# Kernel tuning notes

Hardware: AMD Instinct MI355X
Metric: run time of the kernel (lower is better)

## Reference

```python
import jax, jax.numpy as jnp
import numpy as np

B, T, D_MODEL, N_HEADS = 2, 2048, 1024, 16
HEAD_DIM = D_MODEL // N_HEADS


def _ln(x, g, b, eps=1e-5):
    m = x.mean(-1, keepdims=True)
    v = ((x - m) ** 2).mean(-1, keepdims=True)
    return (x - m) / jnp.sqrt(v + eps) * g + b


def setup_inputs() -> dict:
    key = jax.random.key(0)
    ks = jax.random.split(key, 7)
    f = jnp.float32
    x = jax.random.normal(ks[0], (B, T, D_MODEL), f)
    Wq = jax.random.normal(ks[1], (D_MODEL, D_MODEL), f) * 0.02
    Wk = jax.random.normal(ks[2], (D_MODEL, D_MODEL), f) * 0.02
    Wv = jax.random.normal(ks[3], (D_MODEL, D_MODEL), f) * 0.02
    Wo = jax.random.normal(ks[4], (D_MODEL, D_MODEL), f) * 0.02
    return {
        'x': x, 'Wq': Wq, 'Wk': Wk, 'Wv': Wv, 'Wo': Wo,
        'evolution_rate': jnp.asarray(0.1, f),
        'memory_decay': jnp.asarray(0.85, f),
        'temporal_weights': jax.random.normal(ks[5], (HEAD_DIM,), f) * 0.02,
        'q_gamma': jnp.ones((HEAD_DIM,), f), 'q_beta': jnp.zeros((HEAD_DIM,), f),
        'k_gamma': jnp.ones((HEAD_DIM,), f), 'k_beta': jnp.zeros((HEAD_DIM,), f),
    }


def reference(x, Wq, Wk, Wv, Wo, evolution_rate, memory_decay,
              temporal_weights, q_gamma, q_beta, k_gamma, k_beta):
    b, t, c = x.shape
    h, d = N_HEADS, HEAD_DIM
    # projections (torch Linear: y = x @ W^T), split heads -> [B,H,T,D]
    q = jnp.einsum('btc,oc->bto', x, Wq).reshape(b, t, h, d).transpose(0, 2, 1, 3)
    k = jnp.einsum('btc,oc->bto', x, Wk).reshape(b, t, h, d).transpose(0, 2, 1, 3)
    v = jnp.einsum('btc,oc->bto', x, Wv).reshape(b, t, h, d).transpose(0, 2, 1, 3)

    sig_md = jax.nn.sigmoid(memory_decay)
    # temporal signal per position: sin(sigmoid(er)*(pos+1) * w)  -> [T,D]
    ef = jax.nn.sigmoid(evolution_rate) * jnp.arange(1, t + 1, dtype=x.dtype)
    ts = jnp.sin(ef[:, None] * temporal_weights[None, :])

    def step(mem, inp):  # mem: [B,H,D]
        q_t, k_t, ts_t = inp  # [B,H,D],[B,H,D],[D]
        eq = _ln(q_t + ts_t + sig_md * mem, q_gamma, q_beta)
        ek = _ln(k_t + 0.5 * ts_t + 0.3 * sig_md * mem, k_gamma, k_beta)
        return 0.7 * mem + 0.3 * q_t, (eq, ek)

    mem0 = jnp.zeros((b, h, d), x.dtype)
    qT = q.transpose(2, 0, 1, 3)  # [T,B,H,D]
    kT = k.transpose(2, 0, 1, 3)
    _, (eqT, ekT) = jax.lax.scan(step, mem0, (qT, kT, ts))
    eq = eqT.transpose(1, 2, 0, 3)  # [B,H,T,D]
    ek = ekT.transpose(1, 2, 0, 3)

    scale = 1.0 / np.sqrt(d).astype(np.float32)
    scores = jnp.einsum('bhtd,bhsd->bhts', eq, ek) * scale
    causal = jnp.tril(jnp.ones((t, t), bool))
    scores = jnp.where(causal[None, None], scores, -jnp.inf)
    w = jax.nn.softmax(scores, axis=-1)  # dropout is identity (eval)
    out = jnp.einsum('bhts,bhsd->bhtd', w, v)
    out = out.transpose(0, 2, 1, 3).reshape(b, t, c)
    return jnp.einsum('btc,oc->bto', out, Wo)
```

## Files before the change

### kernel.cpp

```cpp
#include <hip/hip_runtime.h>
#include <stdint.h>

#define T_SEQ   2048
#define NHEADS  16
#define HDIM    64
#define DMODEL  1024

typedef __attribute__((ext_vector_type(8))) _Float16 half8_t;
typedef __attribute__((ext_vector_type(4))) float    float4_t;

typedef __attribute__((address_space(1))) unsigned char ga_u8;
typedef __attribute__((address_space(3))) unsigned char lds_u8;

__device__ __forceinline__ unsigned short f2h(float f) {
  _Float16 h = (_Float16)f;
  return __builtin_bit_cast(unsigned short, h);
}
__device__ __forceinline__ unsigned packh2(float a, float b) {
  return (unsigned)f2h(a) | ((unsigned)f2h(b) << 16);
}
__device__ __forceinline__ unsigned packu2(unsigned short a, unsigned short b) {
  return (unsigned)a | ((unsigned)b << 16);
}
__device__ __forceinline__ void async_copy16(const void* g, void* l) {
  __builtin_amdgcn_global_load_lds((ga_u8*)g, (lds_u8*)l, 16, 0, 0);
}

__global__ __launch_bounds__(256) void cvt_f32_f16(const float* __restrict__ s,
                                                   unsigned short* __restrict__ d, int n4) {
  int i = blockIdx.x * 256 + threadIdx.x;
  if (i >= n4) return;
  float4 v = ((const float4*)s)[i];
  ushort4 o;
  o.x = f2h(v.x); o.y = f2h(v.y); o.z = f2h(v.z); o.w = f2h(v.w);
  ((ushort4*)d)[i] = o;
}

__global__ __launch_bounds__(256) void cvt_weights(
    const float* __restrict__ w0, const float* __restrict__ w1,
    const float* __restrict__ w2, const float* __restrict__ w3,
    unsigned short* __restrict__ d0, unsigned short* __restrict__ d1,
    unsigned short* __restrict__ d2, unsigned short* __restrict__ d3, int n4) {
  int i = blockIdx.x * 256 + threadIdx.x;
  if (i >= n4) return;
  const float* s = (blockIdx.y == 0) ? w0 : (blockIdx.y == 1) ? w1 : (blockIdx.y == 2) ? w2 : w3;
  unsigned short* d = (blockIdx.y == 0) ? d0 : (blockIdx.y == 1) ? d1 : (blockIdx.y == 2) ? d2 : d3;
  float4 v = ((const float4*)s)[i];
  ushort4 o;
  o.x = f2h(v.x); o.y = f2h(v.y); o.z = f2h(v.z); o.w = f2h(v.w);
  ((ushort4*)d)[i] = o;
}

__device__ __forceinline__ void storeC(float* p, float v) { *p = v; }
__device__ __forceinline__ void storeC(unsigned short* p, float v) { *p = f2h(v); }

template <typename OutT>
__global__ __launch_bounds__(256) void gemm_nt_f16(const unsigned short* __restrict__ A,
                                                   const unsigned short* __restrict__ B,
                                                   OutT* __restrict__ C) {
  __shared__ alignas(16) unsigned short As[128 * 32];
  __shared__ alignas(16) unsigned short Bs[128 * 32];
  const int tid  = threadIdx.x;
  const int lane = tid & 63, w = tid >> 6;
  const int c = lane & 15, g = lane >> 4;
  const int wr = w >> 1, wc = w & 1;
  const int m0 = blockIdx.y * 128, n0 = blockIdx.x * 128;

  float4_t acc[4][4];
#pragma unroll
  for (int m = 0; m < 4; ++m)
#pragma unroll
    for (int n = 0; n < 4; ++n) acc[m][n] = (float4_t){0.f, 0.f, 0.f, 0.f};

  for (int k0 = 0; k0 < 1024; k0 += 32) {
    __syncthreads();
#pragma unroll
    for (int r = 0; r < 2; ++r) {
      const int idx = r * 256 + tid;
      const int row = idx >> 2, kc = (idx & 3) * 8;
      async_copy16(A + (size_t)(m0 + row) * 1024 + k0 + kc, As + r * 2048 + w * 512);
      async_copy16(B + (size_t)(n0 + row) * 1024 + k0 + kc, Bs + r * 2048 + w * 512);
    }
    __syncthreads();
    half8_t af[4], bf[4];
#pragma unroll
    for (int m = 0; m < 4; ++m) af[m] = *(const half8_t*)&As[(wr * 64 + m * 16 + c) * 32 + g * 8];
#pragma unroll
    for (int n = 0; n < 4; ++n) bf[n] = *(const half8_t*)&Bs[(wc * 64 + n * 16 + c) * 32 + g * 8];
#pragma unroll
    for (int m = 0; m < 4; ++m)
#pragma unroll
      for (int n = 0; n < 4; ++n)
        acc[m][n] = __builtin_amdgcn_mfma_f32_16x16x32_f16(af[m], bf[n], acc[m][n], 0, 0, 0);
  }
#pragma unroll
  for (int m = 0; m < 4; ++m)
#pragma unroll
    for (int j = 0; j < 4; ++j) {
      const int row = m0 + wr * 64 + m * 16 + g * 4 + j;
#pragma unroll
      for (int n = 0; n < 4; ++n) {
        const int col = n0 + wc * 64 + n * 16 + c;
        storeC(C + (size_t)row * 1024 + col, acc[m][n][j]);
      }
    }
}

__global__ __launch_bounds__(64) void evolve_ln_f32(
    const float* __restrict__ q, const float* __restrict__ k,
    const float* __restrict__ er_p, const float* __restrict__ md_p,
    const float* __restrict__ tw, const float* __restrict__ qgamma,
    const float* __restrict__ qbeta, const float* __restrict__ kgamma,
    const float* __restrict__ kbeta,
    unsigned short* __restrict__ eq, unsigned short* __restrict__ ek) {
  const int lane = threadIdx.x;
  const int t0 = blockIdx.x * 32;
  const int bh = blockIdx.y;
  const int b = bh >> 4, h = bh & 15;
  const float sig_er = 1.f / (1.f + expf(-er_p[0]));
  const float smd    = 1.f / (1.f + expf(-md_p[0]));
  const float wv = tw[lane];
  const float gq = qgamma[lane], bq = qbeta[lane];
  const float gk = kgamma[lane], bk = kbeta[lane];
  const size_t base = ((size_t)b * T_SEQ) * DMODEL + h * HDIM + lane;

  float mem = 0.f;
  const int start = (t0 >= 64) ? (t0 - 64) : 0;
  for (int t = start; t < t0; ++t)
    mem = 0.7f * mem + 0.3f * q[base + (size_t)t * DMODEL];

  for (int t = t0; t < t0 + 32; ++t) {
    const float qv = q[base + (size_t)t * DMODEL];
    const float kv = k[base + (size_t)t * DMODEL];
    const float ts = sinf(sig_er * (float)(t + 1) * wv);
    const float xq = qv + ts + smd * mem;
    const float xk = kv + 0.5f * ts + 0.3f * smd * mem;
    float s1 = xq, s2 = xq * xq, s3 = xk, s4 = xk * xk;
#pragma unroll
    for (int off = 32; off > 0; off >>= 1) {
      s1 += __shfl_xor(s1, off);
      s2 += __shfl_xor(s2, off);
      s3 += __shfl_xor(s3, off);
      s4 += __shfl_xor(s4, off);
    }
    const float mq = s1 * (1.f / 64.f);
    const float vq = fmaxf(s2 * (1.f / 64.f) - mq * mq, 0.f);
    const float mk = s3 * (1.f / 64.f);
    const float vk = fmaxf(s4 * (1.f / 64.f) - mk * mk, 0.f);
    eq[base + (size_t)t * DMODEL] = f2h((xq - mq) * rsqrtf(vq + 1e-5f) * gq + bq);
    ek[base + (size_t)t * DMODEL] = f2h((xk - mk) * rsqrtf(vk + 1e-5f) * gk + bk);
    mem = 0.7f * mem + 0.3f * qv;
  }
}

__global__ __launch_bounds__(256) void attn_fused(
    const unsigned short* __restrict__ eq, const unsigned short* __restrict__ ek,
    const unsigned short* __restrict__ v, unsigned short* __restrict__ o) {
  __shared__ alignas(16) float Ssh[4][16][36];
  __shared__ float Alds[4][16];
  __shared__ float Llds[4][16];
  const int tid = threadIdx.x;
  const int lane = tid & 63, w = tid >> 6;
  const int c = lane & 15, g = lane >> 4;
  const int p = blockIdx.x * 4 + w;
  const int bh = blockIdx.y;
  const int b = bh >> 4, h = bh & 15;
  const size_t head = ((size_t)b * T_SEQ) * DMODEL + h * HDIM;

  for (int half = 0; half < 2; ++half) {
    const int sub = half ? (127 - p) : p;
    const int qw = sub * 16;
    const int qrow = qw + c;

    const half8_t aq0 = *(const half8_t*)(eq + head + (size_t)qrow * DMODEL + g * 8);
    const half8_t aq1 = *(const half8_t*)(eq + head + (size_t)qrow * DMODEL + 32 + g * 8);

    float4_t acc[4];
#pragma unroll
    for (int n = 0; n < 4; ++n) acc[n] = (float4_t){0.f, 0.f, 0.f, 0.f};
    float mrun = -1e30f, lsum = 0.f;

    const int ntiles = (qw >> 5) + 1;
    for (int tile = 0; tile < ntiles; ++tile) {
      const int s0 = tile * 32;
#pragma unroll
      for (int st = 0; st < 2; ++st) {
        const unsigned short* ekr = ek + head + (size_t)(s0 + st * 16 + c) * DMODEL;
        const half8_t bk0 = *(const half8_t*)(ekr + g * 8);
        const half8_t bk1 = *(const half8_t*)(ekr + 32 + g * 8);
        float4_t z = (float4_t){0.f, 0.f, 0.f, 0.f};
        z = __builtin_amdgcn_mfma_f32_16x16x32_f16(aq0, bk0, z, 0, 0, 0);
        z = __builtin_amdgcn_mfma_f32_16x16x32_f16(aq1, bk1, z, 0, 0, 0);
#pragma unroll
        for (int j = 0; j < 4; ++j)
          Ssh[w][g * 4 + j][st * 16 + c] = z[j] * 0.125f;
      }

      float pf[8];
      float tmax = -1e30f;
#pragma unroll
      for (int e = 0; e < 8; ++e) {
        const int sa = s0 + g * 8 + e;
        const float val = (sa <= qrow) ? Ssh[w][c][g * 8 + e] : -1e30f;
        pf[e] = val;
        tmax = fmaxf(tmax, val);
      }
      tmax = fmaxf(tmax, __shfl_xor(tmax, 16));
      tmax = fmaxf(tmax, __shfl_xor(tmax, 32));
      const float mnew = fmaxf(mrun, tmax);
      const float alpha = __expf(mrun - mnew);
      mrun = mnew;
      float psum = 0.f;
#pragma unroll
      for (int e = 0; e < 8; ++e) {
        pf[e] = __expf(pf[e] - mnew);
        psum += pf[e];
      }
      psum += __shfl_xor(psum, 16);
      psum += __shfl_xor(psum, 32);
      lsum = lsum * alpha + psum;
      if (g == 0) Alds[w][c] = alpha;

      uint4 pu;
      pu.x = packh2(pf[0], pf[1]);
      pu.y = packh2(pf[2], pf[3]);
      pu.z = packh2(pf[4], pf[5]);
      pu.w = packh2(pf[6], pf[7]);
      const half8_t pa = __builtin_bit_cast(half8_t, pu);

      float af[4];
#pragma unroll
      for (int j = 0; j < 4; ++j) af[j] = Alds[w][g * 4 + j];
#pragma unroll
      for (int n = 0; n < 4; ++n) {
        acc[n][0] *= af[0]; acc[n][1] *= af[1];
        acc[n][2] *= af[2]; acc[n][3] *= af[3];
      }
      const unsigned short* vp = v + head + (size_t)(s0 + g * 8) * DMODEL + c;
#pragma unroll
      for (int n = 0; n < 4; ++n) {
        const unsigned short* vq2 = vp + n * 16;
        uint4 bu;
        bu.x = packu2(vq2[0 * DMODEL], vq2[1 * DMODEL]);
        bu.y = packu2(vq2[2 * DMODEL], vq2[3 * DMODEL]);
        bu.z = packu2(vq2[4 * DMODEL], vq2[5 * DMODEL]);
        bu.w = packu2(vq2[6 * DMODEL], vq2[7 * DMODEL]);
        const half8_t bv = __builtin_bit_cast(half8_t, bu);
        acc[n] = __builtin_amdgcn_mfma_f32_16x16x32_f16(pa, bv, acc[n], 0, 0, 0);
      }
    }

    if (g == 0) Llds[w][c] = lsum;
    float lj[4];
#pragma unroll
    for (int j = 0; j < 4; ++j) lj[j] = 1.f / Llds[w][g * 4 + j];
#pragma unroll
    for (int n = 0; n < 4; ++n)
#pragma unroll
      for (int j = 0; j < 4; ++j)
        o[head + (size_t)(qw + g * 4 + j) * DMODEL + n * 16 + c] = f2h(acc[n][j] * lj[j]);
  }
}

extern "C" void kernel_launch(void* const* d_in, const int* in_sizes, int n_in,
                              void* d_out, int out_size, void* d_ws, size_t ws_size,
                              hipStream_t stream) {
  const float* x  = (const float*)d_in[0];
  const float* Wq = (const float*)d_in[1];
  const float* Wk = (const float*)d_in[2];
  const float* Wv = (const float*)d_in[3];
  const float* Wo = (const float*)d_in[4];
  const float* er = (const float*)d_in[5];
  const float* md = (const float*)d_in[6];
  const float* tw = (const float*)d_in[7];
  const float* qg = (const float*)d_in[8];
  const float* qb = (const float*)d_in[9];
  const float* kg = (const float*)d_in[10];
  const float* kb = (const float*)d_in[11];

  const size_t NX = (size_t)2 * T_SEQ * DMODEL;
  const size_t NW = (size_t)DMODEL * DMODEL;

  unsigned short* xh  = (unsigned short*)d_ws;
  unsigned short* woh = xh + NX;
  unsigned short* wqh = woh + NW;
  unsigned short* wkh = wqh + NW;
  unsigned short* wvh = wkh + NW;
  float* qf  = (float*)(wvh + NW);
  float* kf  = qf + NX;
  unsigned short* ekh = (unsigned short*)(kf + NX);
  unsigned short* vh  = ekh + NX;
  unsigned short* eqh = xh;
  unsigned short* aoh = (unsigned short*)kf;

  const int n4x = (int)(NX / 4), n4w = (int)(NW / 4);

  cvt_f32_f16<<<n4x / 256, 256, 0, stream>>>(x, xh, n4x);
  cvt_weights<<<dim3(n4w / 256, 4), 256, 0, stream>>>(Wq, Wk, Wv, Wo,
                                                      wqh, wkh, wvh, woh, n4w);

  dim3 ggrid(DMODEL / 128, (2 * T_SEQ) / 128);
  gemm_nt_f16<float><<<ggrid, 256, 0, stream>>>(xh, wqh, qf);
  gemm_nt_f16<float><<<ggrid, 256, 0, stream>>>(xh, wkh, kf);
  gemm_nt_f16<unsigned short><<<ggrid, 256, 0, stream>>>(xh, wvh, vh);

  evolve_ln_f32<<<dim3(T_SEQ / 32, 32), 64, 0, stream>>>(qf, kf, er, md, tw,
                                                         qg, qb, kg, kb, eqh, ekh);

  attn_fused<<<dim3(16, 32), 256, 0, stream>>>(eqh, ekh, vh, aoh);

  gemm_nt_f16<float><<<ggrid, 256, 0, stream>>>(aoh, woh, (float*)d_out);
}
```

Baseline: 252.3 us.

## Pre-transpose V and widen attention KV tiles to 64

Adds a kernel that transposes V per head into a [D,T] layout, so the attention PV MFMA operand loads become contiguous 16-byte vector loads instead of eight strided scalar gathers. It also doubles the KV tile from 32 to 64 keys, halving the softmax rescale and reduction overhead per key. The cost is an extra kernel launch and one extra pass over V in memory, plus higher register and LDS use per wave.

```diff
diff --git a/kernel.cpp b/kernel.cpp
--- a/kernel.cpp
+++ b/kernel.cpp
@@ -153,10 +153,42 @@
   }
 }
 
+__global__ __launch_bounds__(256) void transpose_v(const unsigned short* __restrict__ v,
+                                                   unsigned short* __restrict__ vt) {
+  __shared__ alignas(16) unsigned short tile[64][72];
+  const int tid = threadIdx.x;
+  const int t0 = blockIdx.x * 64;
+  const int bh = blockIdx.y;
+  const int b = bh >> 4, h = bh & 15;
+  const size_t src = ((size_t)b * T_SEQ + t0) * DMODEL + h * HDIM;
+
+  const int r = tid >> 2, c0 = (tid & 3) * 16;
+  const int sw = ((r >> 4) & 3) << 4;
+  const uint4 a0 = *(const uint4*)(v + src + (size_t)r * DMODEL + c0);
+  const uint4 a1 = *(const uint4*)(v + src + (size_t)r * DMODEL + c0 + 8);
+  *(uint4*)&tile[r][c0 ^ sw] = a0;
+  *(uint4*)&tile[r][(c0 ^ sw) + 8] = a1;
+  __syncthreads();
+
+  const int dr = tid >> 2, tc = (tid & 3) * 16;
+  const int swr = ((tc >> 4) & 3) << 4;
+  unsigned short tmp[16];
+#pragma unroll
+  for (int j = 0; j < 16; ++j) tmp[j] = tile[tc + j][dr ^ swr];
+  uint4 o0, o1;
+  o0.x = packu2(tmp[0], tmp[1]);   o0.y = packu2(tmp[2], tmp[3]);
+  o0.z = packu2(tmp[4], tmp[5]);   o0.w = packu2(tmp[6], tmp[7]);
+  o1.x = packu2(tmp[8], tmp[9]);   o1.y = packu2(tmp[10], tmp[11]);
+  o1.z = packu2(tmp[12], tmp[13]); o1.w = packu2(tmp[14], tmp[15]);
+  const size_t dst = (size_t)bh * HDIM * T_SEQ + (size_t)dr * T_SEQ + t0 + tc;
+  *(uint4*)(vt + dst) = o0;
+  *(uint4*)(vt + dst + 8) = o1;
+}
+
 __global__ __launch_bounds__(256) void attn_fused(
     const unsigned short* __restrict__ eq, const unsigned short* __restrict__ ek,
-    const unsigned short* __restrict__ v, unsigned short* __restrict__ o) {
-  __shared__ alignas(16) float Ssh[4][16][36];
+    const unsigned short* __restrict__ vt, unsigned short* __restrict__ o) {
+  __shared__ alignas(16) float Ssh[4][16][68];
   __shared__ float Alds[4][16];
   __shared__ float Llds[4][16];
   const int tid = threadIdx.x;
@@ -165,7 +197,8 @@
   const int p = blockIdx.x * 4 + w;
   const int bh = blockIdx.y;
   const int b = bh >> 4, h = bh & 15;
-  const size_t head = ((size_t)b * T_SEQ) * DMODEL + h * HDIM;
+  const size_t head  = ((size_t)b * T_SEQ) * DMODEL + h * HDIM;
+  const size_t headt = (size_t)bh * HDIM * T_SEQ;
 
   for (int half = 0; half < 2; ++half) {
     const int sub = half ? (127 - p) : p;
@@ -180,11 +213,11 @@
     for (int n = 0; n < 4; ++n) acc[n] = (float4_t){0.f, 0.f, 0.f, 0.f};
     float mrun = -1e30f, lsum = 0.f;
 
-    const int ntiles = (qw >> 5) + 1;
+    const int ntiles = (qw >> 6) + 1;
     for (int tile = 0; tile < ntiles; ++tile) {
-      const int s0 = tile * 32;
-#pragma unroll
-      for (int st = 0; st < 2; ++st) {
+      const int s0 = tile * 64;
+#pragma unroll
+      for (int st = 0; st < 4; ++st) {
         const unsigned short* ekr = ek + head + (size_t)(s0 + st * 16 + c) * DMODEL;
         const half8_t bk0 = *(const half8_t*)(ekr + g * 8);
         const half8_t bk1 = *(const half8_t*)(ekr + 32 + g * 8);
@@ -196,14 +229,16 @@
           Ssh[w][g * 4 + j][st * 16 + c] = z[j] * 0.125f;
       }
 
-      float pf[8];
+      float pf[16];
       float tmax = -1e30f;
 #pragma unroll
       for (int e = 0; e < 8; ++e) {
-        const int sa = s0 + g * 8 + e;
-        const float val = (sa <= qrow) ? Ssh[w][c][g * 8 + e] : -1e30f;
-        pf[e] = val;
-        tmax = fmaxf(tmax, val);
+        const int sa0 = s0 + g * 8 + e;
+        const int sa1 = sa0 + 32;
+        const float v0 = (sa0 <= qrow) ? Ssh[w][c][g * 8 + e] : -1e30f;
+        const float v1 = (sa1 <= qrow) ? Ssh[w][c][32 + g * 8 + e] : -1e30f;
+        pf[e] = v0; pf[8 + e] = v1;
+        tmax = fmaxf(tmax, fmaxf(v0, v1));
       }
       tmax = fmaxf(tmax, __shfl_xor(tmax, 16));
       tmax = fmaxf(tmax, __shfl_xor(tmax, 32));
@@ -212,7 +247,7 @@
       mrun = mnew;
       float psum = 0.f;
 #pragma unroll
-      for (int e = 0; e < 8; ++e) {
+      for (int e = 0; e < 16; ++e) {
         pf[e] = __expf(pf[e] - mnew);
         psum += pf[e];
       }
@@ -221,12 +256,13 @@
       lsum = lsum * alpha + psum;
       if (g == 0) Alds[w][c] = alpha;
 
-      uint4 pu;
-      pu.x = packh2(pf[0], pf[1]);
-      pu.y = packh2(pf[2], pf[3]);
-      pu.z = packh2(pf[4], pf[5]);
-      pu.w = packh2(pf[6], pf[7]);
-      const half8_t pa = __builtin_bit_cast(half8_t, pu);
+      uint4 pu0, pu1;
+      pu0.x = packh2(pf[0], pf[1]);   pu0.y = packh2(pf[2], pf[3]);
+      pu0.z = packh2(pf[4], pf[5]);   pu0.w = packh2(pf[6], pf[7]);
+      pu1.x = packh2(pf[8], pf[9]);   pu1.y = packh2(pf[10], pf[11]);
+      pu1.z = packh2(pf[12], pf[13]); pu1.w = packh2(pf[14], pf[15]);
+      const half8_t pa0 = __builtin_bit_cast(half8_t, pu0);
+      const half8_t pa1 = __builtin_bit_cast(half8_t, pu1);
 
       float af[4];
 #pragma unroll
@@ -236,17 +272,13 @@
         acc[n][0] *= af[0]; acc[n][1] *= af[1];
         acc[n][2] *= af[2]; acc[n][3] *= af[3];
       }
-      const unsigned short* vp = v + head + (size_t)(s0 + g * 8) * DMODEL + c;
 #pragma unroll
       for (int n = 0; n < 4; ++n) {
-        const unsigned short* vq2 = vp + n * 16;
-        uint4 bu;
-        bu.x = packu2(vq2[0 * DMODEL], vq2[1 * DMODEL]);
-        bu.y = packu2(vq2[2 * DMODEL], vq2[3 * DMODEL]);
-        bu.z = packu2(vq2[4 * DMODEL], vq2[5 * DMODEL]);
-        bu.w = packu2(vq2[6 * DMODEL], vq2[7 * DMODEL]);
-        const half8_t bv = __builtin_bit_cast(half8_t, bu);
-        acc[n] = __builtin_amdgcn_mfma_f32_16x16x32_f16(pa, bv, acc[n], 0, 0, 0);
+        const unsigned short* vr = vt + headt + (size_t)(n * 16 + c) * T_SEQ + s0;
+        const half8_t bv0 = *(const half8_t*)(vr + g * 8);
+        const half8_t bv1 = *(const half8_t*)(vr + 32 + g * 8);
+        acc[n] = __builtin_amdgcn_mfma_f32_16x16x32_f16(pa0, bv0, acc[n], 0, 0, 0);
+        acc[n] = __builtin_amdgcn_mfma_f32_16x16x32_f16(pa1, bv1, acc[n], 0, 0, 0);
       }
     }
 
@@ -291,6 +323,7 @@
   unsigned short* ekh = (unsigned short*)(kf + NX);
   unsigned short* vh  = ekh + NX;
   unsigned short* eqh = xh;
+  unsigned short* vth = (unsigned short*)qf;
   unsigned short* aoh = (unsigned short*)kf;
 
   const int n4x = (int)(NX / 4), n4w = (int)(NW / 4);
@@ -307,7 +340,9 @@
   evolve_ln_f32<<<dim3(T_SEQ / 32, 32), 64, 0, stream>>>(qf, kf, er, md, tw,
                                                          qg, qb, kg, kb, eqh, ekh);
 
-  attn_fused<<<dim3(16, 32), 256, 0, stream>>>(eqh, ekh, vh, aoh);
+  transpose_v<<<dim3(T_SEQ / 64, 32), 256, 0, stream>>>(vh, vth);
+
+  attn_fused<<<dim3(16, 32), 256, 0, stream>>>(eqh, ekh, vth, aoh);
 
   gemm_nt_f16<float><<<ggrid, 256, 0, stream>>>(aoh, woh, (float*)d_out);
 }
```

Measured after the change: 298.0 us. 18.1% more time.

## Batch QKV GEMMs into one launch, store Q/K in fp16, split attention grid

Applied to the files above, without the earlier changes.

Merges the three projection GEMMs into one launch that uses blockIdx.z to pick the weight, and writes Q and K as fp16 instead of fp32, so evolve_ln reads half the bytes. The attention kernel drops its paired causal-balancing loop: each wave now handles a single 16-row query tile, and the grid is doubled to 32 blocks. This cuts launch count and memory traffic and raises parallelism. The cost is fp16 rounding of Q/K before the LayerNorm and possible load imbalance, since causal tiles now carry unequal work.

```diff
diff --git a/kernel.cpp b/kernel.cpp
--- a/kernel.cpp
+++ b/kernel.cpp
@@ -15,6 +15,9 @@
 __device__ __forceinline__ unsigned short f2h(float f) {
   _Float16 h = (_Float16)f;
   return __builtin_bit_cast(unsigned short, h);
+}
+__device__ __forceinline__ float h2f(unsigned short u) {
+  return (float)__builtin_bit_cast(_Float16, u);
 }
 __device__ __forceinline__ unsigned packh2(float a, float b) {
   return (unsigned)f2h(a) | ((unsigned)f2h(b) << 16);
@@ -51,13 +54,15 @@
   ((ushort4*)d)[i] = o;
 }
 
-__device__ __forceinline__ void storeC(float* p, float v) { *p = v; }
-__device__ __forceinline__ void storeC(unsigned short* p, float v) { *p = f2h(v); }
-
-template <typename OutT>
-__global__ __launch_bounds__(256) void gemm_nt_f16(const unsigned short* __restrict__ A,
-                                                   const unsigned short* __restrict__ B,
-                                                   OutT* __restrict__ C) {
+__global__ __launch_bounds__(256) void gemm_qkv(
+    const unsigned short* __restrict__ A,
+    const unsigned short* __restrict__ Bq, const unsigned short* __restrict__ Bk,
+    const unsigned short* __restrict__ Bv,
+    unsigned short* __restrict__ Cq, unsigned short* __restrict__ Ck,
+    unsigned short* __restrict__ Cv) {
+  const unsigned short* B = (blockIdx.z == 0) ? Bq : (blockIdx.z == 1) ? Bk : Bv;
+  unsigned short*       C = (blockIdx.z == 0) ? Cq : (blockIdx.z == 1) ? Ck : Cv;
+
   __shared__ alignas(16) unsigned short As[128 * 32];
   __shared__ alignas(16) unsigned short Bs[128 * 32];
   const int tid  = threadIdx.x;
@@ -101,13 +106,64 @@
 #pragma unroll
       for (int n = 0; n < 4; ++n) {
         const int col = n0 + wc * 64 + n * 16 + c;
-        storeC(C + (size_t)row * 1024 + col, acc[m][n][j]);
+        C[(size_t)row * 1024 + col] = f2h(acc[m][n][j]);
       }
     }
 }
 
-__global__ __launch_bounds__(64) void evolve_ln_f32(
-    const float* __restrict__ q, const float* __restrict__ k,
+__global__ __launch_bounds__(256) void gemm_nt_out(const unsigned short* __restrict__ A,
+                                                   const unsigned short* __restrict__ B,
+                                                   float* __restrict__ C) {
+  __shared__ alignas(16) unsigned short As[128 * 32];
+  __shared__ alignas(16) unsigned short Bs[128 * 32];
+  const int tid  = threadIdx.x;
+  const int lane = tid & 63, w = tid >> 6;
+  const int c = lane & 15, g = lane >> 4;
+  const int wr = w >> 1, wc = w & 1;
+  const int m0 = blockIdx.y * 128, n0 = blockIdx.x * 128;
+
+  float4_t acc[4][4];
+#pragma unroll
+  for (int m = 0; m < 4; ++m)
+#pragma unroll
+    for (int n = 0; n < 4; ++n) acc[m][n] = (float4_t){0.f, 0.f, 0.f, 0.f};
+
+  for (int k0 = 0; k0 < 1024; k0 += 32) {
+    __syncthreads();
+#pragma unroll
+    for (int r = 0; r < 2; ++r) {
+      const int idx = r * 256 + tid;
+      const int row = idx >> 2, kc = (idx & 3) * 8;
+      async_copy16(A + (size_t)(m0 + row) * 1024 + k0 + kc, As + r * 2048 + w * 512);
+      async_copy16(B + (size_t)(n0 + row) * 1024 + k0 + kc, Bs + r * 2048 + w * 512);
+    }
+    __syncthreads();
+    half8_t af[4], bf[4];
+#pragma unroll
+    for (int m = 0; m < 4; ++m) af[m] = *(const half8_t*)&As[(wr * 64 + m * 16 + c) * 32 + g * 8];
+#pragma unroll
+    for (int n = 0; n < 4; ++n) bf[n] = *(const half8_t*)&Bs[(wc * 64 + n * 16 + c) * 32 + g * 8];
+#pragma unroll
+    for (int m = 0; m < 4; ++m)
+#pragma unroll
+      for (int n = 0; n < 4; ++n)
+        acc[m][n] = __builtin_amdgcn_mfma_f32_16x16x32_f16(af[m], bf[n], acc[m][n], 0, 0, 0);
+  }
+#pragma unroll
+  for (int m = 0; m < 4; ++m)
+#pragma unroll
+    for (int j = 0; j < 4; ++j) {
+      const int row = m0 + wr * 64 + m * 16 + g * 4 + j;
+#pragma unroll
+      for (int n = 0; n < 4; ++n) {
+        const int col = n0 + wc * 64 + n * 16 + c;
+        C[(size_t)row * 1024 + col] = acc[m][n][j];
+      }
+    }
+}
+
+__global__ __launch_bounds__(64) void evolve_ln(
+    const unsigned short* __restrict__ q, const unsigned short* __restrict__ k,
     const float* __restrict__ er_p, const float* __restrict__ md_p,
     const float* __restrict__ tw, const float* __restrict__ qgamma,
     const float* __restrict__ qbeta, const float* __restrict__ kgamma,
@@ -127,11 +183,11 @@
   float mem = 0.f;
   const int start = (t0 >= 64) ? (t0 - 64) : 0;
   for (int t = start; t < t0; ++t)
-    mem = 0.7f * mem + 0.3f * q[base + (size_t)t * DMODEL];
+    mem = 0.7f * mem + 0.3f * h2f(q[base + (size_t)t * DMODEL]);
 
   for (int t = t0; t < t0 + 32; ++t) {
-    const float qv = q[base + (size_t)t * DMODEL];
-    const float kv = k[base + (size_t)t * DMODEL];
+    const float qv = h2f(q[base + (size_t)t * DMODEL]);
+    const float kv = h2f(k[base + (size_t)t * DMODEL]);
     const float ts = sinf(sig_er * (float)(t + 1) * wv);
     const float xq = qv + ts + smd * mem;
     const float xk = kv + 0.5f * ts + 0.3f * smd * mem;
@@ -162,104 +218,101 @@
   const int tid = threadIdx.x;
   const int lane = tid & 63, w = tid >> 6;
   const int c = lane & 15, g = lane >> 4;
-  const int p = blockIdx.x * 4 + w;
+  const int sub = blockIdx.x * 4 + w;
   const int bh = blockIdx.y;
   const int b = bh >> 4, h = bh & 15;
   const size_t head = ((size_t)b * T_SEQ) * DMODEL + h * HDIM;
 
-  for (int half = 0; half < 2; ++half) {
-    const int sub = half ? (127 - p) : p;
-    const int qw = sub * 16;
-    const int qrow = qw + c;
-
-    const half8_t aq0 = *(const half8_t*)(eq + head + (size_t)qrow * DMODEL + g * 8);
-    const half8_t aq1 = *(const half8_t*)(eq + head + (size_t)qrow * DMODEL + 32 + g * 8);
-
-    float4_t acc[4];
-#pragma unroll
-    for (int n = 0; n < 4; ++n) acc[n] = (float4_t){0.f, 0.f, 0.f, 0.f};
-    float mrun = -1e30f, lsum = 0.f;
-
-    const int ntiles = (qw >> 5) + 1;
-    for (int tile = 0; tile < ntiles; ++tile) {
-      const int s0 = tile * 32;
-#pragma unroll
-      for (int st = 0; st < 2; ++st) {
-        const unsigned short* ekr = ek + head + (size_t)(s0 + st * 16 + c) * DMODEL;
-        const half8_t bk0 = *(const half8_t*)(ekr + g * 8);
-        const half8_t bk1 = *(const half8_t*)(ekr + 32 + g * 8);
-        float4_t z = (float4_t){0.f, 0.f, 0.f, 0.f};
-        z = __builtin_amdgcn_mfma_f32_16x16x32_f16(aq0, bk0, z, 0, 0, 0);
-        z = __builtin_amdgcn_mfma_f32_16x16x32_f16(aq1, bk1, z, 0, 0, 0);
-#pragma unroll
-        for (int j = 0; j < 4; ++j)
-          Ssh[w][g * 4 + j][st * 16 + c] = z[j] * 0.125f;
-      }
-
-      float pf[8];
-      float tmax = -1e30f;
-#pragma unroll
-      for (int e = 0; e < 8; ++e) {
-        const int sa = s0 + g * 8 + e;
-        const float val = (sa <= qrow) ? Ssh[w][c][g * 8 + e] : -1e30f;
-        pf[e] = val;
-        tmax = fmaxf(tmax, val);
-      }
-      tmax = fmaxf(tmax, __shfl_xor(tmax, 16));
-      tmax = fmaxf(tmax, __shfl_xor(tmax, 32));
-      const float mnew = fmaxf(mrun, tmax);
-      const float alpha = __expf(mrun - mnew);
-      mrun = mnew;
-      float psum = 0.f;
-#pragma unroll
-      for (int e = 0; e < 8; ++e) {
-        pf[e] = __expf(pf[e] - mnew);
-        psum += pf[e];
-      }
-      psum += __shfl_xor(psum, 16);
-      psum += __shfl_xor(psum, 32);
-      lsum = lsum * alpha + psum;
-      if (g == 0) Alds[w][c] = alpha;
-
-      uint4 pu;
-      pu.x = packh2(pf[0], pf[1]);
-      pu.y = packh2(pf[2], pf[3]);
-      pu.z = packh2(pf[4], pf[5]);
-      pu.w = packh2(pf[6], pf[7]);
-      const half8_t pa = __builtin_bit_cast(half8_t, pu);
-
-      float af[4];
-#pragma unroll
-      for (int j = 0; j < 4; ++j) af[j] = Alds[w][g * 4 + j];
-#pragma unroll
-      for (int n = 0; n < 4; ++n) {
-        acc[n][0] *= af[0]; acc[n][1] *= af[1];
-        acc[n][2] *= af[2]; acc[n][3] *= af[3];
-      }
-      const unsigned short* vp = v + head + (size_t)(s0 + g * 8) * DMODEL + c;
-#pragma unroll
-      for (int n = 0; n < 4; ++n) {
-        const unsigned short* vq2 = vp + n * 16;
-        uint4 bu;
-        bu.x = packu2(vq2[0 * DMODEL], vq2[1 * DMODEL]);
-        bu.y = packu2(vq2[2 * DMODEL], vq2[3 * DMODEL]);
-        bu.z = packu2(vq2[4 * DMODEL], vq2[5 * DMODEL]);
-        bu.w = packu2(vq2[6 * DMODEL], vq2[7 * DMODEL]);
-        const half8_t bv = __builtin_bit_cast(half8_t, bu);
-        acc[n] = __builtin_amdgcn_mfma_f32_16x16x32_f16(pa, bv, acc[n], 0, 0, 0);
-      }
-    }
-
-    if (g == 0) Llds[w][c] = lsum;
-    float lj[4];
-#pragma unroll
-    for (int j = 0; j < 4; ++j) lj[j] = 1.f / Llds[w][g * 4 + j];
-#pragma unroll
-    for (int n = 0; n < 4; ++n)
+  const int qw = sub * 16;
+  const int qrow = qw + c;
+
+  const half8_t aq0 = *(const half8_t*)(eq + head + (size_t)qrow * DMODEL + g * 8);
+  const half8_t aq1 = *(const half8_t*)(eq + head + (size_t)qrow * DMODEL + 32 + g * 8);
+
+  float4_t acc[4];
+#pragma unroll
+  for (int n = 0; n < 4; ++n) acc[n] = (float4_t){0.f, 0.f, 0.f, 0.f};
+  float mrun = -1e30f, lsum = 0.f;
+
+  const int ntiles = (qw >> 5) + 1;
+  for (int tile = 0; tile < ntiles; ++tile) {
+    const int s0 = tile * 32;
+#pragma unroll
+    for (int st = 0; st < 2; ++st) {
+      const unsigned short* ekr = ek + head + (size_t)(s0 + st * 16 + c) * DMODEL;
+      const half8_t bk0 = *(const half8_t*)(ekr + g * 8);
+      const half8_t bk1 = *(const half8_t*)(ekr + 32 + g * 8);
+      float4_t z = (float4_t){0.f, 0.f, 0.f, 0.f};
+      z = __builtin_amdgcn_mfma_f32_16x16x32_f16(aq0, bk0, z, 0, 0, 0);
+      z = __builtin_amdgcn_mfma_f32_16x16x32_f16(aq1, bk1, z, 0, 0, 0);
 #pragma unroll
       for (int j = 0; j < 4; ++j)
-        o[head + (size_t)(qw + g * 4 + j) * DMODEL + n * 16 + c] = f2h(acc[n][j] * lj[j]);
+        Ssh[w][g * 4 + j][st * 16 + c] = z[j] * 0.125f;
+    }
+
+    float pf[8];
+    float tmax = -1e30f;
+#pragma unroll
+    for (int e = 0; e < 8; ++e) {
+      const int sa = s0 + g * 8 + e;
+      const float val = (sa <= qrow) ? Ssh[w][c][g * 8 + e] : -1e30f;
+      pf[e] = val;
+      tmax = fmaxf(tmax, val);
+    }
+    tmax = fmaxf(tmax, __shfl_xor(tmax, 16));
+    tmax = fmaxf(tmax, __shfl_xor(tmax, 32));
+    const float mnew = fmaxf(mrun, tmax);
+    const float alpha = __expf(mrun - mnew);
+    mrun = mnew;
+    float psum = 0.f;
+#pragma unroll
+    for (int e = 0; e < 8; ++e) {
+      pf[e] = __expf(pf[e] - mnew);
+      psum += pf[e];
+    }
+    psum += __shfl_xor(psum, 16);
+    psum += __shfl_xor(psum, 32);
+    lsum = lsum * alpha + psum;
+    if (g == 0) Alds[w][c] = alpha;
+
+    uint4 pu;
+    pu.x = packh2(pf[0], pf[1]);
+    pu.y = packh2(pf[2], pf[3]);
+    pu.z = packh2(pf[4], pf[5]);
+    pu.w = packh2(pf[6], pf[7]);
+    const half8_t pa = __builtin_bit_cast(half8_t, pu);
+
+    float af[4];
+#pragma unroll
+    for (int j = 0; j < 4; ++j) af[j] = Alds[w][g * 4 + j];
+#pragma unroll
+    for (int n = 0; n < 4; ++n) {
+      acc[n][0] *= af[0]; acc[n][1] *= af[1];
+      acc[n][2] *= af[2]; acc[n][3] *= af[3];
+    }
+    const unsigned short* vp = v + head + (size_t)(s0 + g * 8) * DMODEL + c;
+#pragma unroll
+    for (int n = 0; n < 4; ++n) {
+      const unsigned short* vq2 = vp + n * 16;
+      uint4 bu;
+      bu.x = packu2(vq2[0 * DMODEL], vq2[1 * DMODEL]);
+      bu.y = packu2(vq2[2 * DMODEL], vq2[3 * DMODEL]);
+      bu.z = packu2(vq2[4 * DMODEL], vq2[5 * DMODEL]);
+      bu.w = packu2(vq2[6 * DMODEL], vq2[7 * DMODEL]);
+      const half8_t bv = __builtin_bit_cast(half8_t, bu);
+      acc[n] = __builtin_amdgcn_mfma_f32_16x16x32_f16(pa, bv, acc[n], 0, 0, 0);
+    }
   }
+
+  if (g == 0) Llds[w][c] = lsum;
+  float lj[4];
+#pragma unroll
+  for (int j = 0; j < 4; ++j) lj[j] = 1.f / Llds[w][g * 4 + j];
+#pragma unroll
+  for (int n = 0; n < 4; ++n)
+#pragma unroll
+    for (int j = 0; j < 4; ++j)
+      o[head + (size_t)(qw + g * 4 + j) * DMODEL + n * 16 + c] = f2h(acc[n][j] * lj[j]);
 }
 
 extern "C" void kernel_launch(void* const* d_in, const int* in_sizes, int n_in,
@@ -286,12 +339,12 @@
   unsigned short* wqh = woh + NW;
   unsigned short* wkh = wqh + NW;
   unsigned short* wvh = wkh + NW;
-  float* qf  = (float*)(wvh + NW);
-  float* kf  = qf + NX;
-  unsigned short* ekh = (unsigned short*)(kf + NX);
-  unsigned short* vh  = ekh + NX;
+  unsigned short* qh  = wvh + NW;
+  unsigned short* kh  = qh + NX;
+  unsigned short* vh  = kh + NX;
+  unsigned short* ekh = vh + NX;
+  unsigned short* aoh = ekh + NX;
   unsigned short* eqh = xh;
-  unsigned short* aoh = (unsigned short*)kf;
 
   const int n4x = (int)(NX / 4), n4w = (int)(NW / 4);
 
@@ -300,14 +353,12 @@
                                                       wqh, wkh, wvh, woh, n4w);
 
   dim3 ggrid(DMODEL / 128, (2 * T_SEQ) / 128);
-  gemm_nt_f16<float><<<ggrid, 256, 0, stream>>>(xh, wqh, qf);
-  gemm_nt_f16<float><<<ggrid, 256, 0, stream>>>(xh, wkh, kf);
-  gemm_nt_f16<unsigned short><<<ggrid, 256, 0, stream>>>(xh, wvh, vh);
-
-  evolve_ln_f32<<<dim3(T_SEQ / 32, 32), 64, 0, stream>>>(qf, kf, er, md, tw,
-                                                         qg, qb, kg, kb, eqh, ekh);
-
-  attn_fused<<<dim3(16, 32), 256, 0, stream>>>(eqh, ekh, vh, aoh);
-
-  gemm_nt_f16<float><<<ggrid, 256, 0, stream>>>(aoh, woh, (float*)d_out);
-}
+  gemm_qkv<<<dim3(8, 32, 3), 256, 0, stream>>>(xh, wqh, wkh, wvh, qh, kh, vh);
+
+  evolve_ln<<<dim3(T_SEQ / 32, 32), 64, 0, stream>>>(qh, kh, er, md, tw,
+                                                     qg, qb, kg, kb, eqh, ekh);
+
+  attn_fused<<<dim3(32, 32), 256, 0, stream>>>(eqh, ekh, vh, aoh);
+
+  gemm_nt_out<<<ggrid, 256, 0, stream>>>(aoh, woh, (float*)d_out);
+}
```

Measured after the change: 305.0 us. +20.8%, slower.
